# Performance work log

Measured on AMD Instinct MI355X. Metric: run time of the kernel, lower is better.

## Reference

```python
import jax, jax.numpy as jnp
import numpy as np

B, NNZ = 2048, 8
CAT_V, HVEC_V = 10000, 50000
SYN, SEM = 128, 256
HIDDEN, OUT = 1024, 10000


def setup_inputs() -> dict:
    key = jax.random.key(0)
    ks = jax.random.split(key, 12)
    d_onehot = jax.nn.one_hot(jax.random.randint(ks[0], (B,), 0, 7), 7, dtype=jnp.float32)
    cat_b_ix = jax.random.randint(ks[1], (B,), 0, CAT_V)
    hvb_ix = jax.random.randint(ks[2], (B, NNZ), 0, HVEC_V)
    hvf_ix = jax.random.randint(ks[3], (B, NNZ), 0, HVEC_V)
    hvb_top = jax.random.normal(ks[4], (B, SEM), dtype=jnp.float32)
    hvf_top = jax.random.normal(ks[5], (B, SEM), dtype=jnp.float32)
    cat_embeds = jax.random.normal(ks[6], (CAT_V, SYN), dtype=jnp.float32) * 0.02
    hvec_embeds = jax.random.normal(ks[7], (HVEC_V, SEM), dtype=jnp.float32) * 0.02
    in_dim = 7 + SYN + 2 * SEM
    W1 = jax.random.normal(ks[8], (HIDDEN, in_dim), dtype=jnp.float32) / np.sqrt(in_dim)
    b1 = jnp.zeros((HIDDEN,), dtype=jnp.float32)
    W2 = jax.random.normal(ks[9], (OUT, HIDDEN), dtype=jnp.float32) / np.sqrt(HIDDEN)
    b2 = jnp.zeros((OUT,), dtype=jnp.float32)
    return {"d_onehot": d_onehot, "cat_b_ix": cat_b_ix, "hvb_ix": hvb_ix,
            "hvf_ix": hvf_ix, "hvb_top": hvb_top, "hvf_top": hvf_top,
            "cat_embeds": cat_embeds, "hvec_embeds": hvec_embeds,
            "W1": W1, "b1": b1, "W2": W2, "b2": b2}


def _multi_hot(ix, vocab):
    # set-to-1 semantics: duplicates within a row still yield 1 (matches torch loop)
    rows = jnp.arange(ix.shape[0])[:, None]
    return jnp.zeros((ix.shape[0], vocab), dtype=jnp.float32).at[rows, ix].set(1.0)


def reference(d_onehot, cat_b_ix, hvb_ix, hvf_ix, hvb_top, hvf_top,
              cat_embeds, hvec_embeds, W1, b1, W2, b2):
    cat_b_embed = cat_embeds[cat_b_ix]                      # (B, SYN)
    hvb_mat = _multi_hot(hvb_ix, hvec_embeds.shape[0])      # (B, HVEC_V)
    hvf_mat = _multi_hot(hvf_ix, hvec_embeds.shape[0])
    hvb_embed = hvb_mat @ hvec_embeds + hvb_top             # (B, SEM)
    hvf_embed = hvf_mat @ hvec_embeds + hvf_top
    x = jnp.concatenate([cat_b_embed, hvb_embed, hvf_embed, d_onehot], axis=1)
    x = jax.nn.relu(x @ W1.T + b1)
    x = x @ W2.T + b2
    return jax.nn.log_softmax(x, axis=1)
```

## Files before the change

kernel.cpp:

```cpp
#include <hip/hip_runtime.h>

#define B_      2048
#define SYN     128
#define SEM     256
#define IN_DIM  647
#define K1      704
#define HIDDEN  1024
#define OUT_N   10000
#define NNZ     8

typedef __bf16 bf16x8 __attribute__((ext_vector_type(8)));
typedef float  f32x4  __attribute__((ext_vector_type(4)));
typedef __attribute__((address_space(3))) const unsigned short* lds_cp;

__device__ __forceinline__ unsigned short f2b(float v) {
    __bf16 b = (__bf16)v;
    return __builtin_bit_cast(unsigned short, b);
}

#define NB_W1 2816
#define NB_W2 5000
__global__ __launch_bounds__(256) void prep_light(
    const float* __restrict__ W1,  unsigned short* __restrict__ W1b,
    const float* __restrict__ d_onehot,
    const int*   __restrict__ cat_ix,
    const int*   __restrict__ hvb_ix,
    const int*   __restrict__ hvf_ix,
    const float* __restrict__ hvb_top,
    const float* __restrict__ hvf_top,
    const float* __restrict__ cat_embeds,
    const float* __restrict__ hvec_embeds,
    unsigned short* __restrict__ xb)
{
    const int bb = blockIdx.x, t = threadIdx.x;
    if (bb < NB_W1) {
        int idx = bb * 256 + t;
        int r = idx / K1, c = idx - r * K1;
        W1b[idx] = f2b(c < IN_DIM ? W1[r * IN_DIM + c] : 0.f);
        return;
    }
    const int b = bb - NB_W1;
    unsigned short* xrow = xb + (size_t)b * K1;
    if (t < SYN) {
        int c = cat_ix[b];
        xrow[t] = f2b(cat_embeds[(size_t)c * SYN + t]);
    }
    {
        int ix[NNZ];
        #pragma unroll
        for (int j = 0; j < NNZ; ++j) ix[j] = hvb_ix[b * NNZ + j];
        float s = hvb_top[(size_t)b * SEM + t];
        #pragma unroll
        for (int j = 0; j < NNZ; ++j) {
            bool dup = false;
            for (int k2 = 0; k2 < j; ++k2) dup = dup || (ix[j] == ix[k2]);
            if (!dup) s += hvec_embeds[(size_t)ix[j] * SEM + t];
        }
        xrow[SYN + t] = f2b(s);
    }
    {
        int ix[NNZ];
        #pragma unroll
        for (int j = 0; j < NNZ; ++j) ix[j] = hvf_ix[b * NNZ + j];
        float s = hvf_top[(size_t)b * SEM + t];
        #pragma unroll
        for (int j = 0; j < NNZ; ++j) {
            bool dup = false;
            for (int k2 = 0; k2 < j; ++k2) dup = dup || (ix[j] == ix[k2]);
            if (!dup) s += hvec_embeds[(size_t)ix[j] * SEM + t];
        }
        xrow[SYN + SEM + t] = f2b(s);
    }
    if (t < 7)       xrow[640 + t] = f2b(d_onehot[b * 7 + t]);
    else if (t < 64) xrow[640 + t] = 0;
}

__global__ __launch_bounds__(256) void mid(
    const unsigned short* __restrict__ A,
    const unsigned short* __restrict__ Bm,
    const float* __restrict__ bias,
    unsigned short* __restrict__ H,
    const float* __restrict__ W2,
    unsigned short* __restrict__ W2b)
{
    if (blockIdx.x >= 256) {
        size_t i = (size_t)(blockIdx.x - 256) * 256 + threadIdx.x;
        const float4* src = (const float4*)(W2 + i * 8);
        float4 a = src[0], b = src[1];
        ushort u[8] = { f2b(a.x), f2b(a.y), f2b(a.z), f2b(a.w),
                        f2b(b.x), f2b(b.y), f2b(b.z), f2b(b.w) };
        *(uint4*)(W2b + i * 8) = *(const uint4*)u;
        return;
    }

    constexpr int NI = 2, nt = K1 / 32, K = K1, ncols = HIDDEN, nbm1 = HIDDEN - 1;
    __shared__ __align__(16) unsigned short lds_a[4][128 * 32];
    __shared__ __align__(16) unsigned short lds_b[4][64 * 32];

    const int tid = threadIdx.x;
    const int wv = tid >> 6, ln = tid & 63;
    const int wr = wv >> 1, wc = wv & 1;
    const int lr = ln & 15, lh = ln >> 4;

    const int vbid = blockIdx.x;
    const int nw  = (vbid & 7) * 32 + (vbid >> 3);
    const int mt  = nw % 16, ntile = nw / 16;
    const int m0  = mt * 128, n0 = ntile * 64;

    const unsigned short* srcA[2];
    const unsigned short* srcB[1];
    #pragma unroll
    for (int i = 0; i < 2; ++i) {
        int c = tid + i * 256;
        int row = c >> 2, colL = (((c & 3) ^ ((c >> 3) & 3)) << 3);
        srcA[i] = A + (size_t)(m0 + row) * K + colL;
    }
    {
        int c = tid;
        int row = c >> 2, colL = (((c & 3) ^ ((c >> 3) & 3)) << 3);
        int gr = n0 + row; if (gr > nbm1) gr = nbm1;
        srcB[0] = Bm + (size_t)gr * K + colL;
    }

    auto stage = [&](int buf, int kt) {
        #pragma unroll
        for (int i = 0; i < 2; ++i)
            __builtin_amdgcn_global_load_lds(
                (__attribute__((address_space(1))) const void*)(srcA[i] + kt),
                (__attribute__((address_space(3))) void*)&lds_a[buf][(tid + i * 256) * 8], 16, 0, 0);
        __builtin_amdgcn_global_load_lds(
            (__attribute__((address_space(1))) const void*)(srcB[0] + kt),
            (__attribute__((address_space(3))) void*)&lds_b[buf][tid * 8], 16, 0, 0);
    };

    int a_off[4], b_off[NI];
    #pragma unroll
    for (int mi = 0; mi < 4; ++mi) {
        int row = wr * 64 + mi * 16 + lr;
        a_off[mi] = (row * 64 + lh * 16) ^ (((row >> 1) & 3) << 4);
    }
    #pragma unroll
    for (int ni = 0; ni < NI; ++ni) {
        int row = wc * 32 + ni * 16 + lr;
        b_off[ni] = (row * 64 + lh * 16) ^ (((row >> 1) & 3) << 4);
    }

    f32x4 acc[4][NI];
    {
        f32x4 z = {0.f, 0.f, 0.f, 0.f};
        #pragma unroll
        for (int i = 0; i < 4; ++i)
            #pragma unroll
            for (int j = 0; j < NI; ++j) acc[i][j] = z;
    }

    auto frag_read = [&](bf16x8 (&af)[4], bf16x8 (&bfv)[NI], int buf) {
        lds_cp pa = (lds_cp)&lds_a[buf][0];
        lds_cp pb = (lds_cp)&lds_b[buf][0];
        #pragma unroll
        for (int mi = 0; mi < 4; ++mi) {
            unsigned ad = (unsigned)(unsigned long long)pa + a_off[mi];
            asm volatile("ds_read_b128 %0, %1" : "=v"(af[mi]) : "v"(ad));
        }
        #pragma unroll
        for (int ni = 0; ni < NI; ++ni) {
            unsigned ad = (unsigned)(unsigned long long)pb + b_off[ni];
            asm volatile("ds_read_b128 %0, %1" : "=v"(bfv[ni]) : "v"(ad));
        }
    };
    auto do_mfma = [&](bf16x8 (&af)[4], bf16x8 (&bfv)[NI]) {
        #pragma unroll
        for (int mi = 0; mi < 4; ++mi)
            #pragma unroll
            for (int ni = 0; ni < NI; ++ni)
                acc[mi][ni] = __builtin_amdgcn_mfma_f32_16x16x32_bf16(af[mi], bfv[ni], acc[mi][ni], 0, 0, 0);
    };
    auto do_part = [&](bf16x8 (&rA)[4], bf16x8 (&rB)[NI],
                       bf16x8 (&mA)[4], bf16x8 (&mB)[NI], int p) {
        frag_read(rA, rB, (p + 1) & 3);
        int tp = p + 3; if (tp > nt - 1) tp = nt - 1;
        stage((p + 3) & 3, tp * 32);
        asm volatile("s_waitcnt lgkmcnt(6)" ::: "memory");
        __builtin_amdgcn_sched_barrier(0);
        __builtin_amdgcn_s_setprio(1);
        do_mfma(mA, mB);
        __builtin_amdgcn_s_setprio(0);
        asm volatile("s_waitcnt vmcnt(3)" ::: "memory");
        __builtin_amdgcn_s_barrier();
    };

    stage(0, 0);
    stage(1, 32);
    stage(2, 64);
    asm volatile("s_waitcnt vmcnt(3)" ::: "memory");
    __builtin_amdgcn_s_barrier();

    bf16x8 afX[4], bfX[NI], afY[4], bfY[NI];
    frag_read(afX, bfX, 0);

    for (int t = 0; t < nt; t += 2) {
        do_part(afY, bfY, afX, bfX, t);
        do_part(afX, bfX, afY, bfY, t + 1);
    }

    #pragma unroll
    for (int mi = 0; mi < 4; ++mi) {
        int row = m0 + wr * 64 + mi * 16 + lh * 4;
        #pragma unroll
        for (int ni = 0; ni < NI; ++ni) {
            int col = n0 + wc * 32 + ni * 16 + lr;
            float bb = bias[col];
            #pragma unroll
            for (int r = 0; r < 4; ++r)
                H[(size_t)(row + r) * ncols + col] = f2b(fmaxf(acc[mi][ni][r] + bb, 0.f));
        }
    }
}

template<int NI, int MODE>
__global__ __launch_bounds__(256) void gemm_rt(
    const unsigned short* __restrict__ A,
    const unsigned short* __restrict__ Bm,
    const float* __restrict__ bias,
    void* __restrict__ outp,
    int K, int nt, int ncols, int nbm1, int nm)
{
    constexpr int BN    = 32 * NI;
    constexpr int NB_CH = NI / 2;
    __shared__ __align__(16) unsigned short lds_a[4][128 * 32];
    __shared__ __align__(16) unsigned short lds_b[4][BN * 32];

    const int tid = threadIdx.x;
    const int wv = tid >> 6, ln = tid & 63;
    const int wr = wv >> 1, wc = wv & 1;
    const int lr = ln & 15, lh = ln >> 4;

    const int g   = gridDim.x;
    const int nw  = (blockIdx.x & 7) * (g >> 3) + (blockIdx.x >> 3);
    const int mt  = nw % nm, ntile = nw / nm;
    const int m0  = mt * 128, n0 = ntile * BN;

    const unsigned short* srcA[2];
    const unsigned short* srcB[NB_CH];
    #pragma unroll
    for (int i = 0; i < 2; ++i) {
        int c = tid + i * 256;
        int row = c >> 2, colL = (((c & 3) ^ ((c >> 3) & 3)) << 3);
        srcA[i] = A + (size_t)(m0 + row) * K + colL;
    }
    #pragma unroll
    for (int j = 0; j < NB_CH; ++j) {
        int c = tid + j * 256;
        int row = c >> 2, colL = (((c & 3) ^ ((c >> 3) & 3)) << 3);
        int gr = n0 + row; if (gr > nbm1) gr = nbm1;
        srcB[j] = Bm + (size_t)gr * K + colL;
    }

    auto stage = [&](int buf, int kt) {
        #pragma unroll
        for (int i = 0; i < 2; ++i)
            __builtin_amdgcn_global_load_lds(
                (__attribute__((address_space(1))) const void*)(srcA[i] + kt),
                (__attribute__((address_space(3))) void*)&lds_a[buf][(tid + i * 256) * 8], 16, 0, 0);
        #pragma unroll
        for (int j = 0; j < NB_CH; ++j)
            __builtin_amdgcn_global_load_lds(
                (__attribute__((address_space(1))) const void*)(srcB[j] + kt),
                (__attribute__((address_space(3))) void*)&lds_b[buf][(tid + j * 256) * 8], 16, 0, 0);
    };

    int a_off[4], b_off[NI];
    #pragma unroll
    for (int mi = 0; mi < 4; ++mi) {
        int row = wr * 64 + mi * 16 + lr;
        a_off[mi] = (row * 64 + lh * 16) ^ (((row >> 1) & 3) << 4);
    }
    #pragma unroll
    for (int ni = 0; ni < NI; ++ni) {
        int row = wc * 16 * NI + ni * 16 + lr;
        b_off[ni] = (row * 64 + lh * 16) ^ (((row >> 1) & 3) << 4);
    }

    f32x4 acc[4][NI];
    {
        f32x4 z = {0.f, 0.f, 0.f, 0.f};
        #pragma unroll
        for (int i = 0; i < 4; ++i)
            #pragma unroll
            for (int j = 0; j < NI; ++j) acc[i][j] = z;
    }

    auto frag_read = [&](bf16x8 (&af)[4], bf16x8 (&bfv)[NI], int buf) {
        lds_cp pa = (lds_cp)&lds_a[buf][0];
        lds_cp pb = (lds_cp)&lds_b[buf][0];
        #pragma unroll
        for (int mi = 0; mi < 4; ++mi) {
            unsigned ad = (unsigned)(unsigned long long)pa + a_off[mi];
            asm volatile("ds_read_b128 %0, %1" : "=v"(af[mi]) : "v"(ad));
        }
        #pragma unroll
        for (int ni = 0; ni < NI; ++ni) {
            unsigned ad = (unsigned)(unsigned long long)pb + b_off[ni];
            asm volatile("ds_read_b128 %0, %1" : "=v"(bfv[ni]) : "v"(ad));
        }
    };
    auto do_mfma = [&](bf16x8 (&af)[4], bf16x8 (&bfv)[NI]) {
        #pragma unroll
        for (int mi = 0; mi < 4; ++mi)
            #pragma unroll
            for (int ni = 0; ni < NI; ++ni)
                acc[mi][ni] = __builtin_amdgcn_mfma_f32_16x16x32_bf16(af[mi], bfv[ni], acc[mi][ni], 0, 0, 0);
    };
    auto do_part = [&](bf16x8 (&rA)[4], bf16x8 (&rB)[NI],
                       bf16x8 (&mA)[4], bf16x8 (&mB)[NI], int p) {
        frag_read(rA, rB, (p + 1) & 3);
        int tp = p + 3; if (tp > nt - 1) tp = nt - 1;
        stage((p + 3) & 3, tp * 32);
        if constexpr (NI == 4) asm volatile("s_waitcnt lgkmcnt(8)" ::: "memory");
        else                   asm volatile("s_waitcnt lgkmcnt(6)" ::: "memory");
        __builtin_amdgcn_sched_barrier(0);
        __builtin_amdgcn_s_setprio(1);
        do_mfma(mA, mB);
        __builtin_amdgcn_s_setprio(0);
        if constexpr (NI == 4) asm volatile("s_waitcnt vmcnt(4)" ::: "memory");
        else                   asm volatile("s_waitcnt vmcnt(3)" ::: "memory");
        __builtin_amdgcn_s_barrier();
    };

    stage(0, 0);
    stage(1, 32);
    stage(2, 64);
    if constexpr (NI == 4) asm volatile("s_waitcnt vmcnt(4)" ::: "memory");
    else                   asm volatile("s_waitcnt vmcnt(3)" ::: "memory");
    __builtin_amdgcn_s_barrier();

    bf16x8 afX[4], bfX[NI], afY[4], bfY[NI];
    frag_read(afX, bfX, 0);

    for (int t = 0; t < nt; t += 2) {
        do_part(afY, bfY, afX, bfX, t);
        do_part(afX, bfX, afY, bfY, t + 1);
    }

    #pragma unroll
    for (int mi = 0; mi < 4; ++mi) {
        int row = m0 + wr * 64 + mi * 16 + lh * 4;
        #pragma unroll
        for (int ni = 0; ni < NI; ++ni) {
            int col = n0 + wc * 16 * NI + ni * 16 + lr;
            if (col < ncols) {
                float bb = bias[col];
                if (MODE == 0) {
                    unsigned short* H = (unsigned short*)outp;
                    #pragma unroll
                    for (int r = 0; r < 4; ++r)
                        H[(size_t)(row + r) * ncols + col] = f2b(fmaxf(acc[mi][ni][r] + bb, 0.f));
                } else {
                    float* O = (float*)outp;
                    #pragma unroll
                    for (int r = 0; r < 4; ++r)
                        O[(size_t)(row + r) * ncols + col] = acc[mi][ni][r] + bb;
                }
            }
        }
    }
}

__global__ __launch_bounds__(512, 2) void gemm2_m(
    const unsigned short* __restrict__ A,
    const unsigned short* __restrict__ Bm,
    const float* __restrict__ bias,
    unsigned short* __restrict__ H)
{
    __shared__ __align__(16) unsigned short lA[4][8192];
    __shared__ __align__(16) unsigned short lB[4][10240];
    const int tid = threadIdx.x;
    const int wv = tid >> 6, ln = tid & 63;
    const int wr = wv >> 2, wc = wv & 3;
    const int lr = ln & 15, lh = ln >> 4;

    const int nw = (blockIdx.x & 7) * 32 + (blockIdx.x >> 3);
    const int m0 = (nw & 7) * 256;
    const int n0 = (nw >> 3) * 320;

    const unsigned short* srcA[2];
    const unsigned short* srcB[2];
    const unsigned short* srcB2;
    #pragma unroll
    for (int j = 0; j < 2; ++j) {
        int c = j * 512 + tid;
        int row = c >> 2, colL = (((c & 3) ^ ((c >> 3) & 3)) << 3);
        srcA[j] = A + (size_t)(m0 + row) * HIDDEN + colL;
        int gr = n0 + row; if (gr > OUT_N - 1) gr = OUT_N - 1;
        srcB[j] = Bm + (size_t)gr * HIDDEN + colL;
    }
    const int c2 = 1024 + (wv & 3) * 64 + ln;
    {
        int row = c2 >> 2, colL = (((c2 & 3) ^ ((c2 >> 3) & 3)) << 3);
        int gr = n0 + row; if (gr > OUT_N - 1) gr = OUT_N - 1;
        srcB2 = Bm + (size_t)gr * HIDDEN + colL;
    }

    auto stageA = [&](int slot, int kt) {
        #pragma unroll
        for (int j = 0; j < 2; ++j)
            __builtin_amdgcn_global_load_lds(
                (__attribute__((address_space(1))) const void*)(srcA[j] + kt),
                (__attribute__((address_space(3))) void*)&lA[slot][(j * 512 + tid) * 8], 16, 0, 0);
    };
    auto stageB = [&](int slot, int kt) {
        #pragma unroll
        for (int j = 0; j < 2; ++j)
            __builtin_amdgcn_global_load_lds(
                (__attribute__((address_space(1))) const void*)(srcB[j] + kt),
                (__attribute__((address_space(3))) void*)&lB[slot][(j * 512 + tid) * 8], 16, 0, 0);
        __builtin_amdgcn_global_load_lds(
            (__attribute__((address_space(1))) const void*)(srcB2 + kt),
            (__attribute__((address_space(3))) void*)&lB[slot][c2 * 8], 16, 0, 0);
    };

    int a_off[8], b_off[5];
    #pragma unroll
    for (int mi = 0; mi < 8; ++mi) {
        int row = wr * 128 + mi * 16 + lr;
        a_off[mi] = (row * 64 + lh * 16) ^ (((row >> 1) & 3) << 4);
    }
    #pragma unroll
    for (int ni = 0; ni < 5; ++ni) {
        int row = wc * 80 + ni * 16 + lr;
        b_off[ni] = (row * 64 + lh * 16) ^ (((row >> 1) & 3) << 4);
    }

    f32x4 acc[8][5];
    {
        f32x4 z = {0.f, 0.f, 0.f, 0.f};
        #pragma unroll
        for (int i = 0; i < 8; ++i)
            #pragma unroll
            for (int j = 0; j < 5; ++j) acc[i][j] = z;
    }

    stageA(0, 0);  stageB(0, 0);
    stageA(1, 32); stageB(1, 32);
    stageA(2, 64); stageB(2, 64);
    asm volatile("s_waitcnt vmcnt(10)" ::: "memory");
    __builtin_amdgcn_s_barrier();

    for (int t = 0; t < 32; ++t) {
        const int slot = t & 3;
        const int wsl  = (t + 3) & 3;
        int tp = t + 3; if (tp > 31) tp = 31;
        lds_cp pA = (lds_cp)&lA[slot][0];
        lds_cp pB = (lds_cp)&lB[slot][0];
        bf16x8 af[8], bfv[5];

        #pragma unroll
        for (int ni = 0; ni < 5; ++ni) {
            unsigned ad = (unsigned)(unsigned long long)pB + b_off[ni];
            asm volatile("ds_read_b128 %0, %1" : "=v"(bfv[ni]) : "v"(ad));
        }
        #pragma unroll
        for (int mi = 0; mi < 8; ++mi) {
            unsigned ad = (unsigned)(unsigned long long)pA + a_off[mi];
            asm volatile("ds_read_b128 %0, %1" : "=v"(af[mi]) : "v"(ad));
        }
        stageA(wsl, tp * 32);
        stageB(wsl, tp * 32);

        asm volatile("s_waitcnt lgkmcnt(4)" ::: "memory");
        __builtin_amdgcn_sched_barrier(0);
        __builtin_amdgcn_s_setprio(1);
        #pragma unroll
        for (int mi = 0; mi < 4; ++mi)
            #pragma unroll
            for (int ni = 0; ni < 5; ++ni)
                acc[mi][ni] = __builtin_amdgcn_mfma_f32_16x16x32_bf16(af[mi], bfv[ni], acc[mi][ni], 0, 0, 0);
        __builtin_amdgcn_s_setprio(0);

        asm volatile("s_waitcnt lgkmcnt(0)" ::: "memory");
        __builtin_amdgcn_sched_barrier(0);
        __builtin_amdgcn_s_setprio(1);
        #pragma unroll
        for (int mi = 0; mi < 4; ++mi)
            #pragma unroll
            for (int ni = 0; ni < 5; ++ni)
                acc[4 + mi][ni] = __builtin_amdgcn_mfma_f32_16x16x32_bf16(af[4 + mi], bfv[ni], acc[4 + mi][ni], 0, 0, 0);
        __builtin_amdgcn_s_setprio(0);

        asm volatile("s_waitcnt vmcnt(10)" ::: "memory");
        __builtin_amdgcn_s_barrier();
    }

    #pragma unroll
    for (int mi = 0; mi < 8; ++mi) {
        int row = m0 + wr * 128 + mi * 16 + lh * 4;
        #pragma unroll
        for (int ni = 0; ni < 5; ++ni) {
            int col = n0 + wc * 80 + ni * 16 + lr;
            if (col < OUT_N) {
                float bb = bias[col];
                #pragma unroll
                for (int r = 0; r < 4; ++r)
                    H[(size_t)(row + r) * OUT_N + col] = f2b(acc[mi][ni][r] + bb);
            }
        }
    }
}

__global__ __launch_bounds__(256) void lsm_b(const unsigned short* __restrict__ lg,
                                             float* __restrict__ out) {
    __shared__ __align__(16) uint4 rowbuf[1250];
    __shared__ float redm[4], reds[4];
    __shared__ float s_lz;
    const int t = threadIdx.x, wv = t >> 6, ln = t & 63;
    const unsigned short* l = lg + (size_t)blockIdx.x * OUT_N;
    float* o = out + (size_t)blockIdx.x * OUT_N;

    float m = -3.4e38f, s = 0.f;
    for (int i = t; i < 1250; i += 256) {
        uint4 v = ((const uint4*)l)[i];
        rowbuf[i] = v;
        unsigned w[4] = {v.x, v.y, v.z, v.w};
        float f[8];
        #pragma unroll
        for (int j = 0; j < 4; ++j) {
            f[2*j]   = __builtin_bit_cast(float, w[j] << 16);
            f[2*j+1] = __builtin_bit_cast(float, w[j] & 0xffff0000u);
        }
        float cm = fmaxf(fmaxf(fmaxf(f[0], f[1]), fmaxf(f[2], f[3])),
                         fmaxf(fmaxf(f[4], f[5]), fmaxf(f[6], f[7])));
        if (cm > m) { s *= __expf(m - cm); m = cm; }
        #pragma unroll
        for (int j = 0; j < 8; ++j) s += __expf(f[j] - m);
    }
    #pragma unroll
    for (int off = 32; off > 0; off >>= 1) {
        float om = __shfl_xor(m, off, 64);
        float os = __shfl_xor(s, off, 64);
        float nm = fmaxf(m, om);
        s = s * __expf(m - nm) + os * __expf(om - nm);
        m = nm;
    }
    if (ln == 0) { redm[wv] = m; reds[wv] = s; }
    __syncthreads();
    if (t == 0) {
        float gm = fmaxf(fmaxf(redm[0], redm[1]), fmaxf(redm[2], redm[3]));
        float gs = reds[0] * __expf(redm[0] - gm) + reds[1] * __expf(redm[1] - gm)
                 + reds[2] * __expf(redm[2] - gm) + reds[3] * __expf(redm[3] - gm);
        s_lz = gm + logf(gs);
    }
    __syncthreads();
    const float lz = s_lz;

    for (int i = t; i < 1250; i += 256) {
        uint4 v = rowbuf[i];
        unsigned w[4] = {v.x, v.y, v.z, v.w};
        float4 o0, o1;
        o0.x = __builtin_bit_cast(float, w[0] << 16)          - lz;
        o0.y = __builtin_bit_cast(float, w[0] & 0xffff0000u)  - lz;
        o0.z = __builtin_bit_cast(float, w[1] << 16)          - lz;
        o0.w = __builtin_bit_cast(float, w[1] & 0xffff0000u)  - lz;
        o1.x = __builtin_bit_cast(float, w[2] << 16)          - lz;
        o1.y = __builtin_bit_cast(float, w[2] & 0xffff0000u)  - lz;
        o1.z = __builtin_bit_cast(float, w[3] << 16)          - lz;
        o1.w = __builtin_bit_cast(float, w[3] & 0xffff0000u)  - lz;
        ((float4*)o)[2 * i]     = o0;
        ((float4*)o)[2 * i + 1] = o1;
    }
}

__global__ __launch_bounds__(256) void lsm_f(float* __restrict__ out) {
    __shared__ __align__(16) float rowbuf[OUT_N];
    __shared__ float red[8];
    const int t = threadIdx.x, wv = t >> 6, ln = t & 63;
    float* o = out + (size_t)blockIdx.x * OUT_N;

    float mx = -3.4e38f;
    for (int i = t; i < OUT_N / 4; i += 256) {
        float4 v = ((const float4*)o)[i];
        rowbuf[i*4] = v.x; rowbuf[i*4+1] = v.y; rowbuf[i*4+2] = v.z; rowbuf[i*4+3] = v.w;
        mx = fmaxf(fmaxf(mx, fmaxf(v.x, v.y)), fmaxf(v.z, v.w));
    }
    #pragma unroll
    for (int off = 32; off > 0; off >>= 1) mx = fmaxf(mx, __shfl_xor(mx, off, 64));
    if (ln == 0) red[wv] = mx;
    __syncthreads();
    float m4 = fmaxf(fmaxf(red[0], red[1]), fmaxf(red[2], red[3]));

    float s = 0.f;
    for (int i = t; i < OUT_N; i += 256) s += __expf(rowbuf[i] - m4);
    #pragma unroll
    for (int off = 32; off > 0; off >>= 1) s += __shfl_xor(s, off, 64);
    if (ln == 0) red[4 + wv] = s;
    __syncthreads();
    float lz = m4 + logf(red[4] + red[5] + red[6] + red[7]);

    for (int i = t; i < OUT_N / 4; i += 256) {
        float4 v = { rowbuf[i*4] - lz, rowbuf[i*4+1] - lz,
                     rowbuf[i*4+2] - lz, rowbuf[i*4+3] - lz };
        ((float4*)o)[i] = v;
    }
}

extern "C" void kernel_launch(void* const* d_in, const int* in_sizes, int n_in,
                              void* d_out, int out_size, void* d_ws, size_t ws_size,
                              hipStream_t stream) {
    const float* d_onehot    = (const float*)d_in[0];
    const int*   cat_ix      = (const int*)  d_in[1];
    const int*   hvb_ix      = (const int*)  d_in[2];
    const int*   hvf_ix      = (const int*)  d_in[3];
    const float* hvb_top     = (const float*)d_in[4];
    const float* hvf_top     = (const float*)d_in[5];
    const float* cat_embeds  = (const float*)d_in[6];
    const float* hvec_embeds = (const float*)d_in[7];
    const float* W1          = (const float*)d_in[8];
    const float* b1          = (const float*)d_in[9];
    const float* W2          = (const float*)d_in[10];
    const float* b2          = (const float*)d_in[11];
    float* out = (float*)d_out;

    unsigned short* xb  = (unsigned short*)d_ws;
    unsigned short* W1b = xb  + (size_t)B_ * K1;
    unsigned short* hB  = W1b + (size_t)HIDDEN * K1;
    unsigned short* W2b = hB  + (size_t)B_ * HIDDEN;
    unsigned short* lg  = W2b + (size_t)OUT_N * HIDDEN;
    const size_t need = ((size_t)B_*K1 + (size_t)HIDDEN*K1 + (size_t)B_*HIDDEN
                         + (size_t)OUT_N*HIDDEN + (size_t)B_*OUT_N) * 2;
    const bool bf16_logits = (ws_size >= need);

    prep_light<<<dim3(NB_W1 + B_), dim3(256), 0, stream>>>(
        W1, W1b, d_onehot, cat_ix, hvb_ix, hvf_ix,
        hvb_top, hvf_top, cat_embeds, hvec_embeds, xb);
    mid<<<dim3(256 + NB_W2), dim3(256), 0, stream>>>(xb, W1b, b1, hB, W2, W2b);
    if (bf16_logits) {
        gemm2_m<<<dim3(256), dim3(512), 0, stream>>>(hB, W2b, b2, lg);
        lsm_b<<<dim3(B_), dim3(256), 0, stream>>>(lg, out);
    } else {
        gemm_rt<4, 2><<<dim3(16 * 79), dim3(256), 0, stream>>>(
            hB, W2b, b2, (void*)out, HIDDEN, HIDDEN / 32, OUT_N, OUT_N - 1, 16);
        lsm_f<<<dim3(B_), dim3(256), 0, stream>>>(out);
    }
}
```

Before: 97.06 us.

## Fuse W2 fp32-to-bf16 conversion into the second GEMM's B-tile loading

Drops the separate W2 bf16 conversion pass from the mid kernel. The new gemm2_f instead reads fp32 W2 directly into registers, converts it, and writes bf16 to LDS. This removes a full write and re-read of a 20 MB bf16 copy of W2. In exchange the GEMM pipeline shrinks from 4-stage async LDS loads to 2-stage register-staged loads with a full vmcnt(0) wait each iteration. It also reads twice the bytes of W2 per tile, and those reads are repeated across the 8 M-tiles, which may expose more latency.

```diff
diff --git a/kernel.cpp b/kernel.cpp
--- a/kernel.cpp
+++ b/kernel.cpp
@@ -11,6 +11,7 @@
 
 typedef __bf16 bf16x8 __attribute__((ext_vector_type(8)));
 typedef float  f32x4  __attribute__((ext_vector_type(4)));
+typedef unsigned int u32x2 __attribute__((ext_vector_type(2)));
 typedef __attribute__((address_space(3))) const unsigned short* lds_cp;
 
 __device__ __forceinline__ unsigned short f2b(float v) {
@@ -79,20 +80,8 @@
     const unsigned short* __restrict__ A,
     const unsigned short* __restrict__ Bm,
     const float* __restrict__ bias,
-    unsigned short* __restrict__ H,
-    const float* __restrict__ W2,
-    unsigned short* __restrict__ W2b)
+    unsigned short* __restrict__ H)
 {
-    if (blockIdx.x >= 256) {
-        size_t i = (size_t)(blockIdx.x - 256) * 256 + threadIdx.x;
-        const float4* src = (const float4*)(W2 + i * 8);
-        float4 a = src[0], b = src[1];
-        ushort u[8] = { f2b(a.x), f2b(a.y), f2b(a.z), f2b(a.w),
-                        f2b(b.x), f2b(b.y), f2b(b.z), f2b(b.w) };
-        *(uint4*)(W2b + i * 8) = *(const uint4*)u;
-        return;
-    }
-
     constexpr int NI = 2, nt = K1 / 32, K = K1, ncols = HIDDEN, nbm1 = HIDDEN - 1;
     __shared__ __align__(16) unsigned short lds_a[4][128 * 32];
     __shared__ __align__(16) unsigned short lds_b[4][64 * 32];
@@ -108,7 +97,7 @@
     const int m0  = mt * 128, n0 = ntile * 64;
 
     const unsigned short* srcA[2];
-    const unsigned short* srcB[1];
+    const unsigned short* srcB0;
     #pragma unroll
     for (int i = 0; i < 2; ++i) {
         int c = tid + i * 256;
@@ -119,7 +108,7 @@
         int c = tid;
         int row = c >> 2, colL = (((c & 3) ^ ((c >> 3) & 3)) << 3);
         int gr = n0 + row; if (gr > nbm1) gr = nbm1;
-        srcB[0] = Bm + (size_t)gr * K + colL;
+        srcB0 = Bm + (size_t)gr * K + colL;
     }
 
     auto stage = [&](int buf, int kt) {
@@ -129,7 +118,7 @@
                 (__attribute__((address_space(1))) const void*)(srcA[i] + kt),
                 (__attribute__((address_space(3))) void*)&lds_a[buf][(tid + i * 256) * 8], 16, 0, 0);
         __builtin_amdgcn_global_load_lds(
-            (__attribute__((address_space(1))) const void*)(srcB[0] + kt),
+            (__attribute__((address_space(1))) const void*)(srcB0 + kt),
             (__attribute__((address_space(3))) void*)&lds_b[buf][tid * 8], 16, 0, 0);
     };
 
@@ -215,6 +204,175 @@
                 H[(size_t)(row + r) * ncols + col] = f2b(fmaxf(acc[mi][ni][r] + bb, 0.f));
         }
     }
+}
+
+__global__ __launch_bounds__(512) void gemm2_f(
+    const unsigned short* __restrict__ A,
+    const float* __restrict__ Bm,
+    const float* __restrict__ bias,
+    unsigned short* __restrict__ H)
+{
+    __shared__ __align__(16) unsigned short lA[2][8192];
+    __shared__ __align__(16) unsigned short lB[2][10240];
+    const int tid = threadIdx.x;
+    const int wv = tid >> 6, ln = tid & 63;
+    const int wr = wv >> 2, wc = wv & 3;
+    const int lr = ln & 15, lh = ln >> 4;
+
+    const int nw = (blockIdx.x & 7) * 32 + (blockIdx.x >> 3);
+    const int m0 = (nw & 7) * 256;
+    const int n0 = (nw >> 3) * 320;
+
+    const unsigned short* srcA[2];
+    #pragma unroll
+    for (int j = 0; j < 2; ++j) {
+        int c = j * 512 + tid;
+        int row = c >> 2, colL = (((c & 3) ^ ((c >> 3) & 3)) << 3);
+        srcA[j] = A + (size_t)(m0 + row) * HIDDEN + colL;
+    }
+    const float* srcB[5];
+    int bwr_off[5];
+    #pragma unroll
+    for (int j = 0; j < 5; ++j) {
+        int c = j * 512 + tid;
+        int row = c >> 3, l = c & 7;
+        int gr = n0 + row; if (gr > OUT_N - 1) gr = OUT_N - 1;
+        srcB[j] = Bm + (size_t)gr * HIDDEN + l * 4;
+        int sp = (l >> 1) ^ ((row >> 1) & 3);
+        bwr_off[j] = row * 64 + sp * 16 + (l & 1) * 8;
+    }
+
+    auto stageA = [&](int slot, int kt) {
+        #pragma unroll
+        for (int j = 0; j < 2; ++j)
+            __builtin_amdgcn_global_load_lds(
+                (__attribute__((address_space(1))) const void*)(srcA[j] + kt),
+                (__attribute__((address_space(3))) void*)&lA[slot][(j * 512 + tid) * 8], 16, 0, 0);
+    };
+    auto loadB = [&](f32x4 (&br)[5], int kt) {
+        #pragma unroll
+        for (int j = 0; j < 5; ++j)
+            asm volatile("global_load_dwordx4 %0, %1, off"
+                         : "=v"(br[j]) : "v"(srcB[j] + kt));
+    };
+    auto writeB = [&](f32x4 (&br)[5], int slot) {
+        unsigned base = (unsigned)(unsigned long long)(lds_cp)&lB[slot][0];
+        #pragma unroll
+        for (int j = 0; j < 5; ++j) {
+            unsigned lo = (unsigned)f2b(br[j][0]) | ((unsigned)f2b(br[j][1]) << 16);
+            unsigned hi = (unsigned)f2b(br[j][2]) | ((unsigned)f2b(br[j][3]) << 16);
+            u32x2 d = {lo, hi};
+            unsigned ad = base + bwr_off[j];
+            asm volatile("ds_write_b64 %0, %1" :: "v"(ad), "v"(d));
+        }
+    };
+
+    int a_off[8], b_off[5];
+    #pragma unroll
+    for (int mi = 0; mi < 8; ++mi) {
+        int row = wr * 128 + mi * 16 + lr;
+        a_off[mi] = (row * 64 + lh * 16) ^ (((row >> 1) & 3) << 4);
+    }
+    #pragma unroll
+    for (int ni = 0; ni < 5; ++ni) {
+        int row = wc * 80 + ni * 16 + lr;
+        b_off[ni] = (row * 64 + lh * 16) ^ (((row >> 1) & 3) << 4);
+    }
+
+    f32x4 acc[8][5];
+    {
+        f32x4 z = {0.f, 0.f, 0.f, 0.f};
+        #pragma unroll
+        for (int i = 0; i < 8; ++i)
+            #pragma unroll
+            for (int j = 0; j < 5; ++j) acc[i][j] = z;
+    }
+
+    {
+        f32x4 br[5];
+        stageA(0, 0);
+        loadB(br, 0);
+        asm volatile("s_waitcnt vmcnt(0)" ::: "memory");
+        __builtin_amdgcn_sched_barrier(0);
+        writeB(br, 0);
+        asm volatile("s_waitcnt lgkmcnt(0)" ::: "memory");
+        __builtin_amdgcn_s_barrier();
+    }
+
+    for (int t = 0; t < 32; ++t) {
+        const int slot = t & 1;
+        const int wsl  = (t + 1) & 1;
+        int tp = t + 1; if (tp > 31) tp = 31;
+        lds_cp pA = (lds_cp)&lA[slot][0];
+        lds_cp pB = (lds_cp)&lB[slot][0];
+        bf16x8 af[8], bfv[5];
+        f32x4 br[5];
+
+        #pragma unroll
+        for (int ni = 0; ni < 5; ++ni) {
+            unsigned ad = (unsigned)(unsigned long long)pB + b_off[ni];
+            asm volatile("ds_read_b128 %0, %1" : "=v"(bfv[ni]) : "v"(ad));
+        }
+        #pragma unroll
+        for (int mi = 0; mi < 8; ++mi) {
+            unsigned ad = (unsigned)(unsigned long long)pA + a_off[mi];
+            asm volatile("ds_read_b128 %0, %1" : "=v"(af[mi]) : "v"(ad));
+        }
+        stageA(wsl, tp * 32);
+        loadB(br, tp * 32);
+
+        asm volatile("s_waitcnt lgkmcnt(4)" ::: "memory");
+        __builtin_amdgcn_sched_barrier(0);
+        __builtin_amdgcn_s_setprio(1);
+        #pragma unroll
+        for (int mi = 0; mi < 4; ++mi)
+            #pragma unroll
+            for (int ni = 0; ni < 5; ++ni)
+                acc[mi][ni] = __builtin_amdgcn_mfma_f32_16x16x32_bf16(af[mi], bfv[ni], acc[mi][ni], 0, 0, 0);
+        __builtin_amdgcn_s_setprio(0);
+
+        asm volatile("s_waitcnt lgkmcnt(0)" ::: "memory");
+        __builtin_amdgcn_sched_barrier(0);
+        __builtin_amdgcn_s_setprio(1);
+        #pragma unroll
+        for (int mi = 0; mi < 4; ++mi)
+            #pragma unroll
+            for (int ni = 0; ni < 5; ++ni)
+                acc[4 + mi][ni] = __builtin_amdgcn_mfma_f32_16x16x32_bf16(af[4 + mi], bfv[ni], acc[4 + mi][ni], 0, 0, 0);
+        __builtin_amdgcn_s_setprio(0);
+
+        asm volatile("s_waitcnt vmcnt(0)" ::: "memory");
+        __builtin_amdgcn_sched_barrier(0);
+        writeB(br, wsl);
+        asm volatile("s_waitcnt lgkmcnt(0)" ::: "memory");
+        __builtin_amdgcn_s_barrier();
+    }
+
+    #pragma unroll
+    for (int mi = 0; mi < 8; ++mi) {
+        int row = m0 + wr * 128 + mi * 16 + lh * 4;
+        #pragma unroll
+        for (int ni = 0; ni < 5; ++ni) {
+            int col = n0 + wc * 80 + ni * 16 + lr;
+            if (col < OUT_N) {
+                float bb = bias[col];
+                #pragma unroll
+                for (int r = 0; r < 4; ++r)
+                    H[(size_t)(row + r) * OUT_N + col] = f2b(acc[mi][ni][r] + bb);
+            }
+        }
+    }
+}
+
+__global__ __launch_bounds__(256) void cvt_w2(const float* __restrict__ W2,
+                                              unsigned short* __restrict__ W2b) {
+    size_t i = (size_t)blockIdx.x * 256 + threadIdx.x;
+    if (i >= (size_t)OUT_N * HIDDEN / 8) return;
+    const float4* src = (const float4*)(W2 + i * 8);
+    float4 a = src[0], b = src[1];
+    ushort u[8] = { f2b(a.x), f2b(a.y), f2b(a.z), f2b(a.w),
+                    f2b(b.x), f2b(b.y), f2b(b.z), f2b(b.w) };
+    *(uint4*)(W2b + i * 8) = *(const uint4*)u;
 }
 
 template<int NI, int MODE>
@@ -366,147 +524,6 @@
     }
 }
 
-__global__ __launch_bounds__(512, 2) void gemm2_m(
-    const unsigned short* __restrict__ A,
-    const unsigned short* __restrict__ Bm,
-    const float* __restrict__ bias,
-    unsigned short* __restrict__ H)
-{
-    __shared__ __align__(16) unsigned short lA[4][8192];
-    __shared__ __align__(16) unsigned short lB[4][10240];
-    const int tid = threadIdx.x;
-    const int wv = tid >> 6, ln = tid & 63;
-    const int wr = wv >> 2, wc = wv & 3;
-    const int lr = ln & 15, lh = ln >> 4;
-
-    const int nw = (blockIdx.x & 7) * 32 + (blockIdx.x >> 3);
-    const int m0 = (nw & 7) * 256;
-    const int n0 = (nw >> 3) * 320;
-
-    const unsigned short* srcA[2];
-    const unsigned short* srcB[2];
-    const unsigned short* srcB2;
-    #pragma unroll
-    for (int j = 0; j < 2; ++j) {
-        int c = j * 512 + tid;
-        int row = c >> 2, colL = (((c & 3) ^ ((c >> 3) & 3)) << 3);
-        srcA[j] = A + (size_t)(m0 + row) * HIDDEN + colL;
-        int gr = n0 + row; if (gr > OUT_N - 1) gr = OUT_N - 1;
-        srcB[j] = Bm + (size_t)gr * HIDDEN + colL;
-    }
-    const int c2 = 1024 + (wv & 3) * 64 + ln;
-    {
-        int row = c2 >> 2, colL = (((c2 & 3) ^ ((c2 >> 3) & 3)) << 3);
-        int gr = n0 + row; if (gr > OUT_N - 1) gr = OUT_N - 1;
-        srcB2 = Bm + (size_t)gr * HIDDEN + colL;
-    }
-
-    auto stageA = [&](int slot, int kt) {
-        #pragma unroll
-        for (int j = 0; j < 2; ++j)
-            __builtin_amdgcn_global_load_lds(
-                (__attribute__((address_space(1))) const void*)(srcA[j] + kt),
-                (__attribute__((address_space(3))) void*)&lA[slot][(j * 512 + tid) * 8], 16, 0, 0);
-    };
-    auto stageB = [&](int slot, int kt) {
-        #pragma unroll
-        for (int j = 0; j < 2; ++j)
-            __builtin_amdgcn_global_load_lds(
-                (__attribute__((address_space(1))) const void*)(srcB[j] + kt),
-                (__attribute__((address_space(3))) void*)&lB[slot][(j * 512 + tid) * 8], 16, 0, 0);
-        __builtin_amdgcn_global_load_lds(
-            (__attribute__((address_space(1))) const void*)(srcB2 + kt),
-            (__attribute__((address_space(3))) void*)&lB[slot][c2 * 8], 16, 0, 0);
-    };
-
-    int a_off[8], b_off[5];
-    #pragma unroll
-    for (int mi = 0; mi < 8; ++mi) {
-        int row = wr * 128 + mi * 16 + lr;
-        a_off[mi] = (row * 64 + lh * 16) ^ (((row >> 1) & 3) << 4);
-    }
-    #pragma unroll
-    for (int ni = 0; ni < 5; ++ni) {
-        int row = wc * 80 + ni * 16 + lr;
-        b_off[ni] = (row * 64 + lh * 16) ^ (((row >> 1) & 3) << 4);
-    }
-
-    f32x4 acc[8][5];
-    {
-        f32x4 z = {0.f, 0.f, 0.f, 0.f};
-        #pragma unroll
-        for (int i = 0; i < 8; ++i)
-            #pragma unroll
-            for (int j = 0; j < 5; ++j) acc[i][j] = z;
-    }
-
-    stageA(0, 0);  stageB(0, 0);
-    stageA(1, 32); stageB(1, 32);
-    stageA(2, 64); stageB(2, 64);
-    asm volatile("s_waitcnt vmcnt(10)" ::: "memory");
-    __builtin_amdgcn_s_barrier();
-
-    for (int t = 0; t < 32; ++t) {
-        const int slot = t & 3;
-        const int wsl  = (t + 3) & 3;
-        int tp = t + 3; if (tp > 31) tp = 31;
-        lds_cp pA = (lds_cp)&lA[slot][0];
-        lds_cp pB = (lds_cp)&lB[slot][0];
-        bf16x8 af[8], bfv[5];
-
-        #pragma unroll
-        for (int ni = 0; ni < 5; ++ni) {
-            unsigned ad = (unsigned)(unsigned long long)pB + b_off[ni];
-            asm volatile("ds_read_b128 %0, %1" : "=v"(bfv[ni]) : "v"(ad));
-        }
-        #pragma unroll
-        for (int mi = 0; mi < 8; ++mi) {
-            unsigned ad = (unsigned)(unsigned long long)pA + a_off[mi];
-            asm volatile("ds_read_b128 %0, %1" : "=v"(af[mi]) : "v"(ad));
-        }
-        stageA(wsl, tp * 32);
-        stageB(wsl, tp * 32);
-
-        asm volatile("s_waitcnt lgkmcnt(4)" ::: "memory");
-        __builtin_amdgcn_sched_barrier(0);
-        __builtin_amdgcn_s_setprio(1);
-        #pragma unroll
-        for (int mi = 0; mi < 4; ++mi)
-            #pragma unroll
-            for (int ni = 0; ni < 5; ++ni)
-                acc[mi][ni] = __builtin_amdgcn_mfma_f32_16x16x32_bf16(af[mi], bfv[ni], acc[mi][ni], 0, 0, 0);
-        __builtin_amdgcn_s_setprio(0);
-
-        asm volatile("s_waitcnt lgkmcnt(0)" ::: "memory");
-        __builtin_amdgcn_sched_barrier(0);
-        __builtin_amdgcn_s_setprio(1);
-        #pragma unroll
-        for (int mi = 0; mi < 4; ++mi)
-            #pragma unroll
-            for (int ni = 0; ni < 5; ++ni)
-                acc[4 + mi][ni] = __builtin_amdgcn_mfma_f32_16x16x32_bf16(af[4 + mi], bfv[ni], acc[4 + mi][ni], 0, 0, 0);
-        __builtin_amdgcn_s_setprio(0);
-
-        asm volatile("s_waitcnt vmcnt(10)" ::: "memory");
-        __builtin_amdgcn_s_barrier();
-    }
-
-    #pragma unroll
-    for (int mi = 0; mi < 8; ++mi) {
-        int row = m0 + wr * 128 + mi * 16 + lh * 4;
-        #pragma unroll
-        for (int ni = 0; ni < 5; ++ni) {
-            int col = n0 + wc * 80 + ni * 16 + lr;
-            if (col < OUT_N) {
-                float bb = bias[col];
-                #pragma unroll
-                for (int r = 0; r < 4; ++r)
-                    H[(size_t)(row + r) * OUT_N + col] = f2b(acc[mi][ni][r] + bb);
-            }
-        }
-    }
-}
-
 __global__ __launch_bounds__(256) void lsm_b(const unsigned short* __restrict__ lg,
                                              float* __restrict__ out) {
     __shared__ __align__(16) uint4 rowbuf[1250];
@@ -622,20 +639,21 @@
     unsigned short* xb  = (unsigned short*)d_ws;
     unsigned short* W1b = xb  + (size_t)B_ * K1;
     unsigned short* hB  = W1b + (size_t)HIDDEN * K1;
-    unsigned short* W2b = hB  + (size_t)B_ * HIDDEN;
-    unsigned short* lg  = W2b + (size_t)OUT_N * HIDDEN;
+    unsigned short* lg  = hB  + (size_t)B_ * HIDDEN;
     const size_t need = ((size_t)B_*K1 + (size_t)HIDDEN*K1 + (size_t)B_*HIDDEN
-                         + (size_t)OUT_N*HIDDEN + (size_t)B_*OUT_N) * 2;
+                         + (size_t)B_*OUT_N) * 2;
     const bool bf16_logits = (ws_size >= need);
 
     prep_light<<<dim3(NB_W1 + B_), dim3(256), 0, stream>>>(
         W1, W1b, d_onehot, cat_ix, hvb_ix, hvf_ix,
         hvb_top, hvf_top, cat_embeds, hvec_embeds, xb);
-    mid<<<dim3(256 + NB_W2), dim3(256), 0, stream>>>(xb, W1b, b1, hB, W2, W2b);
+    mid<<<dim3(256), dim3(256), 0, stream>>>(xb, W1b, b1, hB);
     if (bf16_logits) {
-        gemm2_m<<<dim3(256), dim3(512), 0, stream>>>(hB, W2b, b2, lg);
+        gemm2_f<<<dim3(256), dim3(512), 0, stream>>>(hB, W2, b2, lg);
         lsm_b<<<dim3(B_), dim3(256), 0, stream>>>(lg, out);
     } else {
+        unsigned short* W2b = lg;
+        cvt_w2<<<dim3((OUT_N * HIDDEN / 8 + 255) / 256), dim3(256), 0, stream>>>(W2, W2b);
         gemm_rt<4, 2><<<dim3(16 * 79), dim3(256), 0, stream>>>(
             hB, W2b, b2, (void*)out, HIDDEN, HIDDEN / 32, OUT_N, OUT_N - 1, 16);
         lsm_f<<<dim3(B_), dim3(256), 0, stream>>>(out);
```

Result: slower. 115.3 us (+18.8%).
